# Kernel tuning notes

Measured on AMD Instinct MI355X. Metric: run time of the kernel, lower is better.

The kernel has to match this reference:

```python
import jax, jax.numpy as jnp
import numpy as np

# constants from init_kwargs (data_info / model_cfg)
FX = 300.0
FY = 300.0
CX = 128.0
CY = 128.0
BG = 1.0            # data_info['bg_color']
EPS2D = 0.3         # gsplat screen-space blur added to 2D covariance diagonal
NEAR = 0.01         # gsplat near-plane cull
C0 = 0.28209479177387814  # SH degree-0 basis
N_PTS = 512
IMG = 256


def quat_to_rotmat(q):
    # q: (N,4) wxyz, normalized inside
    q = q / jnp.linalg.norm(q, axis=-1, keepdims=True)
    w, x, y, z = q[:, 0], q[:, 1], q[:, 2], q[:, 3]
    return jnp.stack([
        jnp.stack([1 - 2 * (y * y + z * z), 2 * (x * y - w * z), 2 * (x * z + w * y)], -1),
        jnp.stack([2 * (x * y + w * z), 1 - 2 * (x * x + z * z), 2 * (y * z - w * x)], -1),
        jnp.stack([2 * (x * z - w * y), 2 * (y * z + w * x), 1 - 2 * (x * x + y * y)], -1),
    ], axis=-2)  # (N,3,3)


def setup_inputs() -> dict:
    key = jax.random.key(0)
    k = jax.random.split(key, 6)
    means = (jax.random.uniform(k[0], (N_PTS, 3), dtype=jnp.float32) - 0.5) * 10.0
    quats = jax.random.normal(k[1], (N_PTS, 4), dtype=jnp.float32)
    # log-scales around 0.2m so Gaussians actually cover pixels
    scales = jnp.log(0.2) + 0.1 * jax.random.normal(k[2], (N_PTS, 3), dtype=jnp.float32)
    opacities = jax.random.normal(k[3], (N_PTS,), dtype=jnp.float32)
    sh0 = 0.5 * jax.random.normal(k[4], (N_PTS, 1, 3), dtype=jnp.float32)
    shN = 0.01 * jax.random.normal(k[5], (N_PTS, 15, 3), dtype=jnp.float32)
    camtoworld = jnp.concatenate([jnp.eye(3, dtype=jnp.float32), jnp.zeros((3, 1), jnp.float32)], axis=1)
    return {"camtoworld": camtoworld, "means": means, "quats": quats, "scales": scales,
            "opacities": opacities, "sh0": sh0, "shN": shN, "img_h": IMG, "img_w": IMG}


def _render(camtoworld, means, quats, scales, opacities, sh0, shN, img_h, img_w):
    # --- camera setup (matches module forward) ---
    c2w = jnp.eye(4, dtype=jnp.float32).at[:3, :].set(camtoworld)
    viewmat = jnp.linalg.inv(c2w)
    viewmat = viewmat.at[1, :].multiply(-1.0).at[2, :].multiply(-1.0)
    R, t = viewmat[:3, :3], viewmat[:3, 3]

    # --- project means ---
    p = means @ R.T + t                      # (N,3) camera-space
    x, y, z = p[:, 0], p[:, 1], p[:, 2]
    valid = z > NEAR
    zs = jnp.where(valid, z, 1.0)
    rz = 1.0 / zs

    # --- 3D covariance: R(q) diag(s^2) R(q)^T, rotated to camera ---
    Rq = quat_to_rotmat(quats)
    M = Rq * jnp.exp(scales)[:, None, :]
    cov3d = M @ jnp.swapaxes(M, 1, 2)        # (N,3,3)
    cov_cam = jnp.einsum('ij,njk,lk->nil', R, cov3d, R)

    # --- EWA perspective Jacobian with fov clipping (gsplat persp_proj) ---
    limx = 1.3 * (0.5 * img_w / FX)
    limy = 1.3 * (0.5 * img_h / FY)
    tx = zs * jnp.clip(x * rz, -limx, limx)
    ty = zs * jnp.clip(y * rz, -limy, limy)
    zero = jnp.zeros_like(rz)
    J = jnp.stack([
        jnp.stack([FX * rz, zero, -FX * tx * rz * rz], -1),
        jnp.stack([zero, FY * rz, -FY * ty * rz * rz], -1),
    ], axis=1)                               # (N,2,3)
    cov2d = jnp.einsum('nij,njk,nlk->nil', J, cov_cam, J)
    a = cov2d[:, 0, 0] + EPS2D
    b = cov2d[:, 0, 1]
    c = cov2d[:, 1, 1] + EPS2D
    det = a * c - b * b
    valid = valid & (det > 1e-12)
    dets = jnp.where(valid, det, 1.0)
    cA, cB, cC = c / dets, -b / dets, a / dets   # conic (inverse 2D covariance)

    mx = FX * x * rz + CX
    my = FY * y * rz + CY

    # --- colors: sh_degree = 0 -> only sh0 band, clamped to >= 0 ---
    color = jnp.maximum(C0 * sh0[:, 0, :] + 0.5, 0.0)   # (N,3)
    opac = jax.nn.sigmoid(opacities)

    # --- depth sort (front to back) ---
    order = jnp.argsort(jnp.where(valid, z, jnp.inf))
    mx, my, cA, cB, cC, opac, color, valid = (v[order] for v in (mx, my, cA, cB, cC, opac, color, valid))

    # --- per-pixel alpha evaluation (dense [N,H,W]) ---
    px = jnp.arange(img_w, dtype=jnp.float32) + 0.5
    py = jnp.arange(img_h, dtype=jnp.float32) + 0.5
    dx = px[None, None, :] - mx[:, None, None]          # (N,H,W)
    dy = py[None, :, None] - my[:, None, None]
    sigma = 0.5 * (cA[:, None, None] * dx * dx + cC[:, None, None] * dy * dy) + cB[:, None, None] * dx * dy
    alpha = jnp.minimum(0.999, opac[:, None, None] * jnp.exp(-sigma))
    alpha = jnp.where((sigma >= 0.0) & (alpha >= 1.0 / 255.0) & valid[:, None, None], alpha, 0.0)

    # --- front-to-back alpha compositing via exclusive cumprod of (1-alpha) ---
    T = jnp.cumprod(1.0 - alpha, axis=0)                # (N,H,W)
    T_excl = jnp.concatenate([jnp.ones_like(T[:1]), T[:-1]], axis=0)
    w = T_excl * alpha
    render = jnp.einsum('nhw,nc->hwc', w, color) + T[-1][..., None] * BG   # (H,W,3)
    alpha_map = (1.0 - T[-1])[..., None]                                   # (H,W,1)
    return render, alpha_map


def reference(camtoworld, means, quats, scales, opacities, sh0, shN, img_h, img_w):
    return _render(camtoworld, means, quats, scales, opacities, sh0, shN, img_h, img_w)
```

## Files before the change

### kernel.cpp

```cpp
#include <hip/hip_runtime.h>
#include <math.h>

#define FXc 300.0f
#define FYc 300.0f
#define CXc 128.0f
#define CYc 128.0f
#define BGc 1.0f
#define EPS2Dc 0.3f
#define NEARc 0.01f
#define C0c 0.28209479177387814f

#define MAXP 512
#define SEG  4

__global__ void __launch_bounds__(1024)
gs_fused(const float* __restrict__ cam,
         const float* __restrict__ means,
         const float* __restrict__ quats,
         const float* __restrict__ scales,
         const float* __restrict__ opacs,
         const float* __restrict__ sh0,
         const int* __restrict__ img_w_p,
         float* __restrict__ out,
         int n, int npix)
{
    __shared__ float4 spts[MAXP][3];
    __shared__ __align__(16) float zc[MAXP + 4];
    __shared__ int scnt[MAXP / 64];
    __shared__ int sbase[MAXP / 64 + 1];
    __shared__ float4 comb[SEG - 1][256];

    const int lt   = threadIdx.x;
    const int wave = lt >> 6, lane = lt & 63;

    const int W = *img_w_p;
    const int tiles_x = W >> 4;
    const int tx = (blockIdx.x % tiles_x) << 4;
    const int ty = (blockIdx.x / tiles_x) << 4;
    const float tx0 = (float)tx + 0.5f, tx1 = (float)tx + 15.5f;
    const float ty0 = (float)ty + 0.5f, ty1 = (float)ty + 15.5f;

    const int nchunks = (n + 63) >> 6;

    float pmx = 0.f, pmy = 0.f, pA_ = 0.f, pB_ = 0.f, pC_ = 0.f;
    float pop = 0.f, pcr = 0.f, pcg = 0.f, pcb = 0.f, pz = 0.f;
    unsigned long long mreg = 0ull;
    bool phit = false;

    if (lt < MAXP) {
        const float a00 = cam[0], a01 = cam[1], a02 = cam[2],  b0 = cam[3];
        const float a10 = cam[4], a11 = cam[5], a12 = cam[6],  b1 = cam[7];
        const float a20 = cam[8], a21 = cam[9], a22 = cam[10], b2 = cam[11];
        const float det3 = a00*(a11*a22 - a12*a21) - a01*(a10*a22 - a12*a20) + a02*(a10*a21 - a11*a20);
        const float id = 1.0f / det3;
        const float i00 = (a11*a22 - a12*a21)*id, i01 = (a02*a21 - a01*a22)*id, i02 = (a01*a12 - a02*a11)*id;
        const float i10 = (a12*a20 - a10*a22)*id, i11 = (a00*a22 - a02*a20)*id, i12 = (a02*a10 - a00*a12)*id;
        const float i20 = (a10*a21 - a11*a20)*id, i21 = (a01*a20 - a00*a21)*id, i22 = (a00*a11 - a01*a10)*id;
        const float R00 = i00,  R01 = i01,  R02 = i02;
        const float R10 = -i10, R11 = -i11, R12 = -i12;
        const float R20 = -i20, R21 = -i21, R22 = -i22;
        const float t0 = -(i00*b0 + i01*b1 + i02*b2);
        const float t1 = (i10*b0 + i11*b1 + i12*b2);
        const float t2 = (i20*b0 + i21*b1 + i22*b2);
        const float limx_e = 1.3f * (0.5f * (float)W / FXc);
        const float limy_e = limx_e;

        const int p = lt;
        bool hit = false;
        if (p < n) {
            const float m0 = means[3*p], m1 = means[3*p+1], m2 = means[3*p+2];
            const float px_ = R00*m0 + R01*m1 + R02*m2 + t0;
            const float py_ = R10*m0 + R11*m1 + R12*m2 + t1;
            const float pz_ = R20*m0 + R21*m1 + R22*m2 + t2;

            bool valid = pz_ > NEARc;
            const float zs = valid ? pz_ : 1.0f;
            const float rz = 1.0f / zs;

            float qw = quats[4*p], qx = quats[4*p+1], qy = quats[4*p+2], qz = quats[4*p+3];
            const float qn = rsqrtf(qw*qw + qx*qx + qy*qy + qz*qz);
            qw *= qn; qx *= qn; qy *= qn; qz *= qn;
            const float Rq00 = 1.f - 2.f*(qy*qy + qz*qz), Rq01 = 2.f*(qx*qy - qw*qz), Rq02 = 2.f*(qx*qz + qw*qy);
            const float Rq10 = 2.f*(qx*qy + qw*qz), Rq11 = 1.f - 2.f*(qx*qx + qz*qz), Rq12 = 2.f*(qy*qz - qw*qx);
            const float Rq20 = 2.f*(qx*qz - qw*qy), Rq21 = 2.f*(qy*qz + qw*qx), Rq22 = 1.f - 2.f*(qx*qx + qy*qy);

            const float e0 = __expf(scales[3*p]), e1 = __expf(scales[3*p+1]), e2 = __expf(scales[3*p+2]);
            const float M00 = Rq00*e0, M01 = Rq01*e1, M02 = Rq02*e2;
            const float M10 = Rq10*e0, M11 = Rq11*e1, M12 = Rq12*e2;
            const float M20 = Rq20*e0, M21 = Rq21*e1, M22 = Rq22*e2;

            const float S00 = M00*M00 + M01*M01 + M02*M02;
            const float S01 = M00*M10 + M01*M11 + M02*M12;
            const float S02 = M00*M20 + M01*M21 + M02*M22;
            const float S11 = M10*M10 + M11*M11 + M12*M12;
            const float S12 = M10*M20 + M11*M21 + M12*M22;
            const float S22 = M20*M20 + M21*M21 + M22*M22;

            const float U00 = R00*S00 + R01*S01 + R02*S02;
            const float U01 = R00*S01 + R01*S11 + R02*S12;
            const float U02 = R00*S02 + R01*S12 + R02*S22;
            const float U10 = R10*S00 + R11*S01 + R12*S02;
            const float U11 = R10*S01 + R11*S11 + R12*S12;
            const float U12 = R10*S02 + R11*S12 + R12*S22;
            const float U20 = R20*S00 + R21*S01 + R22*S02;
            const float U21 = R20*S01 + R21*S11 + R22*S12;
            const float U22 = R20*S02 + R21*S12 + R22*S22;

            const float C00 = U00*R00 + U01*R01 + U02*R02;
            const float C01 = U00*R10 + U01*R11 + U02*R12;
            const float C02 = U00*R20 + U01*R21 + U02*R22;
            const float C11 = U10*R10 + U11*R11 + U12*R12;
            const float C12 = U10*R20 + U11*R21 + U12*R22;
            const float C22 = U20*R20 + U21*R21 + U22*R22;

            const float txc = zs * fminf(fmaxf(px_*rz, -limx_e), limx_e);
            const float tyc = zs * fminf(fmaxf(py_*rz, -limy_e), limy_e);
            const float ja0 = FXc * rz;
            const float ja2 = -FXc * txc * rz * rz;
            const float jb1 = FYc * rz;
            const float jb2 = -FYc * tyc * rz * rz;

            const float c2d00 = ja0*ja0*C00 + 2.f*ja0*ja2*C02 + ja2*ja2*C22 + EPS2Dc;
            const float c2d01 = ja0*jb1*C01 + ja0*jb2*C02 + ja2*jb1*C12 + ja2*jb2*C22;
            const float c2d11 = jb1*jb1*C11 + 2.f*jb1*jb2*C12 + jb2*jb2*C22 + EPS2Dc;

            const float det2 = c2d00*c2d11 - c2d01*c2d01;
            valid = valid && (det2 > 1e-12f);
            const float rdet = 1.0f / (valid ? det2 : 1.0f);
            pA_ = c2d11 * rdet;
            pB_ = -c2d01 * rdet;
            pC_ = c2d00 * rdet;

            pmx = FXc * px_ * rz + CXc;
            pmy = FYc * py_ * rz + CYc;

            pcr = fmaxf(C0c * sh0[3*p+0] + 0.5f, 0.0f);
            pcg = fmaxf(C0c * sh0[3*p+1] + 0.5f, 0.0f);
            pcb = fmaxf(C0c * sh0[3*p+2] + 0.5f, 0.0f);
            pop = 1.0f / (1.0f + __expf(-opacs[p]));
            pz  = pz_;

            const float op255 = pop * 255.0f;
            if (valid && op255 >= 1.0f) {
                const float s = __logf(op255);
                const float dxm = sqrtf(2.0f * s * c2d00) * 1.0001f + 0.01f;
                const float dym = sqrtf(2.0f * s * c2d11) * 1.0001f + 0.01f;
                hit = (pmx - dxm <= tx1) && (pmx + dxm >= tx0) &&
                      (pmy - dym <= ty1) && (pmy + dym >= ty0);
            }
        }
        phit = hit;
        mreg = __ballot(hit);
        if (lane == 0) scnt[wave] = __popcll(mreg);
    }
    __syncthreads();

    if (lt == 0) {
        int acc = 0;
        for (int c = 0; c < nchunks; ++c) { sbase[c] = acc; acc += scnt[c]; }
        sbase[nchunks] = acc;
    }
    __syncthreads();
    const int k = sbase[nchunks];

    int pslot = -1;
    if (lt < MAXP && phit) {
        pslot = sbase[wave] + __popcll(mreg & ((1ull << lane) - 1ull));
        zc[pslot] = pz;
    }
    if (lt < 4) zc[k + lt] = INFINITY;
    __syncthreads();

    if (pslot >= 0) {
        const float za = pz;
        const int sa = pslot;
        int rank = 0;
        const float4* z4 = (const float4*)zc;
        const int k4 = (k + 3) >> 2;
        for (int j4 = 0; j4 < k4; ++j4) {
            const float4 v = z4[j4];
            const int j = j4 << 2;
            rank += (v.x < za || (v.x == za && (j+0) < sa));
            rank += (v.y < za || (v.y == za && (j+1) < sa));
            rank += (v.z < za || (v.z == za && (j+2) < sa));
            rank += (v.w < za || (v.w == za && (j+3) < sa));
        }
        spts[rank][0] = make_float4(pmx, pmy, pA_, pB_);
        spts[rank][1] = make_float4(pC_, pop, pcr, pcg);
        spts[rank][2] = make_float4(pcb, 0.f, 0.f, 0.f);
    }
    __syncthreads();

    const int s   = lt >> 8;
    const int pix = lt & 255;
    const int col = tx + (pix & 15);
    const int row = ty + (pix >> 4);
    const float px = (float)col + 0.5f;
    const float py = (float)row + 0.5f;

    const int beg = (k * s) >> 2;
    const int end = (k * (s + 1)) >> 2;

    float T = 1.0f, r_ = 0.f, g_ = 0.f, b_ = 0.f;
    for (int base = beg; base < end; base += 16) {
        const int lim = (base + 16 < end) ? base + 16 : end;
        #pragma unroll 4
        for (int i = base; i < lim; ++i) {
            const float4 a4 = spts[i][0];
            const float4 b4 = spts[i][1];
            const float  cbv = spts[i][2].x;

            const float dx = px - a4.x;
            const float dy = py - a4.y;
            const float sigma = 0.5f * (a4.z*dx*dx + b4.x*dy*dy) + a4.w*dx*dy;
            float al = b4.y * __expf(-sigma);
            al = fminf(al, 0.999f);
            const bool keep = (sigma >= 0.0f) && (al >= (1.0f/255.0f));
            al = keep ? al : 0.0f;

            const float w = T * al;
            r_ += w * b4.z;
            g_ += w * b4.w;
            b_ += w * cbv;
            T *= (1.0f - al);
        }
        if (!__any(T > 1e-4f)) break;
    }

    if (s > 0) comb[s - 1][pix] = make_float4(r_, g_, b_, T);
    __syncthreads();

    if (s == 0) {
        const float4 f1 = comb[0][pix];
        const float4 f2 = comb[1][pix];
        const float4 f3 = comb[2][pix];
        float rr = r_ + T * (f1.x + f1.w * (f2.x + f2.w * f3.x));
        float gg = g_ + T * (f1.y + f1.w * (f2.y + f2.w * f3.y));
        float bb = b_ + T * (f1.z + f1.w * (f2.z + f2.w * f3.z));
        const float Tt = T * f1.w * f2.w * f3.w;
        rr += Tt * BGc; gg += Tt * BGc; bb += Tt * BGc;

        const int opix = row * W + col;
        if (opix < npix) {
            out[3*opix + 0] = rr;
            out[3*opix + 1] = gg;
            out[3*opix + 2] = bb;
            out[3*npix + opix] = 1.0f - Tt;
        }
    }
}

extern "C" void kernel_launch(void* const* d_in, const int* in_sizes, int n_in,
                              void* d_out, int out_size, void* d_ws, size_t ws_size,
                              hipStream_t stream) {
    const float* cam    = (const float*)d_in[0];
    const float* means  = (const float*)d_in[1];
    const float* quats  = (const float*)d_in[2];
    const float* scales = (const float*)d_in[3];
    const float* opacs  = (const float*)d_in[4];
    const float* sh0    = (const float*)d_in[5];
    const int* img_w = (const int*)d_in[8];

    const int n = in_sizes[4];
    const int npix = out_size / 4;

    const int blocks = npix / 256;
    gs_fused<<<blocks, 1024, 0, stream>>>(cam, means, quats, scales, opacs, sh0,
                                          img_w, (float*)d_out, n, npix);
}
```

Measured before the change: 10.47 us.

## Replace O(k^2) rank-count depth sort with bitonic sort on packed keys

```diff
diff --git a/kernel.cpp b/kernel.cpp
--- a/kernel.cpp
+++ b/kernel.cpp
@@ -25,13 +25,14 @@
          int n, int npix)
 {
     __shared__ float4 spts[MAXP][3];
-    __shared__ __align__(16) float zc[MAXP + 4];
-    __shared__ int scnt[MAXP / 64];
-    __shared__ int sbase[MAXP / 64 + 1];
+    __shared__ unsigned long long keys[MAXP];
+    __shared__ int  srank[MAXP];
+    __shared__ int  scnt[MAXP / 64];
+    __shared__ int  sK;
     __shared__ float4 comb[SEG - 1][256];
 
     const int lt   = threadIdx.x;
-    const int wave = lt >> 6, lane = lt & 63;
+    const int wave = lt >> 6;
 
     const int W = *img_w_p;
     const int tiles_x = W >> 4;
@@ -40,11 +41,8 @@
     const float tx0 = (float)tx + 0.5f, tx1 = (float)tx + 15.5f;
     const float ty0 = (float)ty + 0.5f, ty1 = (float)ty + 15.5f;
 
-    const int nchunks = (n + 63) >> 6;
-
     float pmx = 0.f, pmy = 0.f, pA_ = 0.f, pB_ = 0.f, pC_ = 0.f;
     float pop = 0.f, pcr = 0.f, pcg = 0.f, pcb = 0.f, pz = 0.f;
-    unsigned long long mreg = 0ull;
     bool phit = false;
 
     if (lt < MAXP) {
@@ -150,46 +148,69 @@
             }
         }
         phit = hit;
-        mreg = __ballot(hit);
-        if (lane == 0) scnt[wave] = __popcll(mreg);
-    }
-    __syncthreads();
-
+        const unsigned long long m = __ballot(hit);
+        if ((lt & 63) == 0) scnt[wave] = __popcll(m);
+    }
+
+    unsigned long long key = ~0ull;
+    if (phit) key = ((unsigned long long)__float_as_uint(pz) << 32) | (unsigned)lt;
+
+    __syncthreads();
     if (lt == 0) {
         int acc = 0;
-        for (int c = 0; c < nchunks; ++c) { sbase[c] = acc; acc += scnt[c]; }
-        sbase[nchunks] = acc;
-    }
-    __syncthreads();
-    const int k = sbase[nchunks];
-
-    int pslot = -1;
-    if (lt < MAXP && phit) {
-        pslot = sbase[wave] + __popcll(mreg & ((1ull << lane) - 1ull));
-        zc[pslot] = pz;
-    }
-    if (lt < 4) zc[k + lt] = INFINITY;
-    __syncthreads();
-
-    if (pslot >= 0) {
-        const float za = pz;
-        const int sa = pslot;
-        int rank = 0;
-        const float4* z4 = (const float4*)zc;
-        const int k4 = (k + 3) >> 2;
-        for (int j4 = 0; j4 < k4; ++j4) {
-            const float4 v = z4[j4];
-            const int j = j4 << 2;
-            rank += (v.x < za || (v.x == za && (j+0) < sa));
-            rank += (v.y < za || (v.y == za && (j+1) < sa));
-            rank += (v.z < za || (v.z == za && (j+2) < sa));
-            rank += (v.w < za || (v.w == za && (j+3) < sa));
-        }
-        spts[rank][0] = make_float4(pmx, pmy, pA_, pB_);
-        spts[rank][1] = make_float4(pC_, pop, pcr, pcg);
-        spts[rank][2] = make_float4(pcb, 0.f, 0.f, 0.f);
-    }
-    __syncthreads();
+        #pragma unroll
+        for (int c = 0; c < MAXP/64; ++c) acc += scnt[c];
+        sK = acc;
+    }
+
+    {
+        const bool active = (lt < MAXP);
+        for (int size = 2; size <= 64; size <<= 1) {
+            const bool dir = ((lt & size) == 0);
+            for (int stride = size >> 1; stride > 0; stride >>= 1) {
+                if (active) {
+                    const unsigned long long b = __shfl_xor(key, stride, 64);
+                    const bool lower = ((lt & stride) == 0);
+                    const bool takeMin = (lower == dir);
+                    key = takeMin ? (key < b ? key : b) : (key > b ? key : b);
+                }
+            }
+        }
+        for (int size = 128; size <= MAXP; size <<= 1) {
+            const bool dir = ((lt & size) == 0);
+            for (int stride = size >> 1; stride >= 64; stride >>= 1) {
+                __syncthreads();
+                if (active) keys[lt] = key;
+                __syncthreads();
+                if (active) {
+                    const unsigned long long b = keys[lt ^ stride];
+                    const bool lower = ((lt & stride) == 0);
+                    const bool takeMin = (lower == dir);
+                    key = takeMin ? (key < b ? key : b) : (key > b ? key : b);
+                }
+            }
+            for (int stride = 32; stride > 0; stride >>= 1) {
+                if (active) {
+                    const unsigned long long b = __shfl_xor(key, stride, 64);
+                    const bool lower = ((lt & stride) == 0);
+                    const bool takeMin = (lower == dir);
+                    key = takeMin ? (key < b ? key : b) : (key > b ? key : b);
+                }
+            }
+        }
+    }
+
+    if (lt < MAXP && key != ~0ull) srank[(int)(key & 0xffffffffu)] = lt;
+    __syncthreads();
+
+    if (phit) {
+        const int r = srank[lt];
+        spts[r][0] = make_float4(pmx, pmy, pA_, pB_);
+        spts[r][1] = make_float4(pC_, pop, pcr, pcg);
+        spts[r][2] = make_float4(pcb, 0.f, 0.f, 0.f);
+    }
+    __syncthreads();
+    const int k = sK;
 
     const int s   = lt >> 8;
     const int pix = lt & 255;
@@ -222,7 +243,7 @@
             r_ += w * b4.z;
             g_ += w * b4.w;
             b_ += w * cbv;
-            T *= (1.0f - al);
+            T = __builtin_fmaf(-al, T, T);
         }
         if (!__any(T > 1e-4f)) break;
     }
```

Measured after the change: 14.35 us. +37.0%, slower.
